# Performance work log

Hardware: AMD Instinct MI355X
Metric: run time of the kernel (lower is better)

Reference implementation:

```python
import jax, jax.numpy as jnp
import numpy as np

N = 50000
E = 640000
D_IN = 128
D_OUT = 128


def setup_inputs() -> dict:
    key = jax.random.key(0)
    k1, k2, k3, k4 = jax.random.split(key, 4)
    x = jax.random.normal(k1, (N, D_IN), dtype=jnp.float32)
    edge_index = jax.random.randint(k2, (2, E), 0, N, dtype=jnp.int64)
    # Linear(in_channels, out_channels) params, PyTorch default init scale
    lim = 1.0 / np.sqrt(D_IN)
    W = jax.random.uniform(k3, (D_IN, D_OUT), dtype=jnp.float32, minval=-lim, maxval=lim)
    b = jax.random.uniform(k4, (D_OUT,), dtype=jnp.float32, minval=-lim, maxval=lim)
    return {"x": x, "edge_index": edge_index, "W": W, "b": b}


def reference(x, edge_index, W, b):
    row, col = edge_index[0], edge_index[1]
    # gather source features, segment-sum onto destination rows
    msgs = x[col]  # [E, D_IN]
    summed = jax.ops.segment_sum(msgs, row, num_segments=N)  # [N, D_IN]
    counts = jax.ops.segment_sum(jnp.ones((E,), dtype=x.dtype), row, num_segments=N)
    # scatter_mean: empty segments -> 0 (avoid div by zero)
    x_agg = summed / jnp.maximum(counts, 1.0)[:, None]
    # Linear + ReLU
    return jax.nn.relu(x_agg @ W + b)
```

## Files before the change

kernel.cpp:

```cpp
#include <hip/hip_runtime.h>

#define NN 50000
#define DD 128
#define PAD 16
#define CAP 48
#define GEMM_BLOCKS 391

typedef __attribute__((ext_vector_type(8))) short bf16x8;
typedef __attribute__((ext_vector_type(4))) float f32x4;

static __device__ __forceinline__ unsigned short f2bf(float x) {
    unsigned int u = __float_as_uint(x);
    unsigned int r = (u + 0x7fffu + ((u >> 16) & 1u)) >> 16;
    return (unsigned short)r;
}

static __device__ __forceinline__ int swz(int byte) {
    return byte ^ (((byte >> 8) & 7) << 4);
}

__global__ void __launch_bounds__(256) zero_wt_kernel(
    int* __restrict__ pad, const float* __restrict__ W, unsigned short* __restrict__ Wt)
{
    if (blockIdx.x == 0) {
        for (int idx = threadIdx.x; idx < DD * DD; idx += 256) {
            int k = idx >> 7;
            int j = idx & 127;
            Wt[j * DD + k] = f2bf(W[idx]);
        }
    }
    int i = blockIdx.x * 256 + threadIdx.x;
    const int total = NN * PAD / 4;
    if (i < total) {
        reinterpret_cast<uint4*>(pad)[i] = make_uint4(0u, 0u, 0u, 0u);
    }
}

__global__ void __launch_bounds__(256) ticket_place_kernel(
    const int* __restrict__ row, const int* __restrict__ col,
    int* __restrict__ pad, unsigned short* __restrict__ slot, int E)
{
    int e = blockIdx.x * 256 + threadIdx.x;
    if (e < E) {
        int r = row[e];
        int t = atomicAdd(&pad[r * PAD], 1);
        if (t < CAP) slot[r * CAP + t] = (unsigned short)col[e];
    }
}

__global__ void __launch_bounds__(512) gemm_xw_kernel(
    const float* __restrict__ x,
    const unsigned short* __restrict__ Wt,
    unsigned short* __restrict__ y)
{
    __shared__ unsigned short w_lds[DD * DD];
    __shared__ unsigned short r_lds[128 * DD];

    const int tid = threadIdx.x;
    const int i0 = blockIdx.x * 128;

    {
        const uint4* src = reinterpret_cast<const uint4*>(Wt);
        #pragma unroll
        for (int it = 0; it < 4; ++it) {
            int idx = tid + it * 512;
            uint4 v = src[idx];
            *reinterpret_cast<uint4*>((char*)w_lds + swz(idx * 16)) = v;
        }
    }

    const int wave = tid >> 6;
    const int l64 = tid & 63;
    const int lrow = l64 & 15;
    const int kgrp = l64 >> 4;
    const int grow = min(i0 + wave * 16 + lrow, NN - 1);

    bf16x8 afrag[4];
    #pragma unroll
    for (int s = 0; s < 4; ++s) {
        const float4* xp = reinterpret_cast<const float4*>(
            x + (size_t)grow * DD + s * 32 + kgrp * 8);
        float4 p0 = xp[0];
        float4 p1 = xp[1];
        bf16x8 a;
        a[0] = (short)f2bf(p0.x); a[1] = (short)f2bf(p0.y);
        a[2] = (short)f2bf(p0.z); a[3] = (short)f2bf(p0.w);
        a[4] = (short)f2bf(p1.x); a[5] = (short)f2bf(p1.y);
        a[6] = (short)f2bf(p1.z); a[7] = (short)f2bf(p1.w);
        afrag[s] = a;
    }
    __syncthreads();

    f32x4 acc[8];
    #pragma unroll
    for (int t = 0; t < 8; ++t) acc[t] = (f32x4){0.f, 0.f, 0.f, 0.f};

    #pragma unroll
    for (int t = 0; t < 8; ++t) {
        #pragma unroll
        for (int s = 0; s < 4; ++s) {
            int byte = (t * 16 + lrow) * 256 + (s * 32 + kgrp * 8) * 2;
            bf16x8 bfrag = *reinterpret_cast<const bf16x8*>((char*)w_lds + swz(byte));
            acc[t] = __builtin_amdgcn_mfma_f32_16x16x32_bf16(afrag[s], bfrag, acc[t], 0, 0, 0);
        }
    }

    #pragma unroll
    for (int t = 0; t < 8; ++t) {
        #pragma unroll
        for (int r = 0; r < 4; ++r) {
            int lr = wave * 16 + kgrp * 4 + r;
            int byte = lr * 256 + (t * 16 + lrow) * 2;
            *reinterpret_cast<unsigned short*>((char*)r_lds + swz(byte)) = f2bf(acc[t][r]);
        }
    }
    __syncthreads();

    {
        uint4* dst = reinterpret_cast<uint4*>(y) + (size_t)i0 * 16;
        #pragma unroll
        for (int it = 0; it < 4; ++it) {
            int idx = tid + it * 512;
            if (i0 + (idx >> 4) < NN) {
                uint4 v = *reinterpret_cast<const uint4*>((char*)r_lds + swz(idx * 16));
                dst[idx] = v;
            }
        }
    }
}

__global__ void __launch_bounds__(256) gather_out_kernel(
    const unsigned short* __restrict__ y,
    const int* __restrict__ pad,
    const unsigned short* __restrict__ slot,
    const float* __restrict__ bias,
    float* __restrict__ out)
{
    int node = blockIdx.x * 8 + (threadIdx.x >> 5);
    int lane = threadIdx.x & 31;
    int q = lane >> 3;
    int l8 = lane & 7;
    if (node >= NN) return;
    int cnt0 = pad[node * PAD];
    int cnt = min(cnt0, CAP);
    int start = node * CAP;
    int end = start + cnt;

    float acc[16];
    #pragma unroll
    for (int j = 0; j < 16; ++j) acc[j] = 0.f;

    for (int base = start; base < end; base += 32) {
        int cl = (base + lane < end) ? (int)slot[base + lane] : 0;
        int m = min(32, end - base);
        for (int ii = 0; ii < m; ii += 4) {
            int src = ii + q;
            int c = __shfl(cl, src, 32);
            if (src < m) {
                const uint4* yp = reinterpret_cast<const uint4*>(y + (size_t)c * DD) + 2 * l8;
                uint4 u0 = yp[0];
                uint4 u1 = yp[1];
                acc[0]  += __uint_as_float(u0.x << 16);
                acc[1]  += __uint_as_float(u0.x & 0xffff0000u);
                acc[2]  += __uint_as_float(u0.y << 16);
                acc[3]  += __uint_as_float(u0.y & 0xffff0000u);
                acc[4]  += __uint_as_float(u0.z << 16);
                acc[5]  += __uint_as_float(u0.z & 0xffff0000u);
                acc[6]  += __uint_as_float(u0.w << 16);
                acc[7]  += __uint_as_float(u0.w & 0xffff0000u);
                acc[8]  += __uint_as_float(u1.x << 16);
                acc[9]  += __uint_as_float(u1.x & 0xffff0000u);
                acc[10] += __uint_as_float(u1.y << 16);
                acc[11] += __uint_as_float(u1.y & 0xffff0000u);
                acc[12] += __uint_as_float(u1.z << 16);
                acc[13] += __uint_as_float(u1.z & 0xffff0000u);
                acc[14] += __uint_as_float(u1.w << 16);
                acc[15] += __uint_as_float(u1.w & 0xffff0000u);
            }
        }
    }
    #pragma unroll
    for (int j = 0; j < 16; ++j) {
        acc[j] += __shfl_xor(acc[j], 8, 32);
        acc[j] += __shfl_xor(acc[j], 16, 32);
    }

    float inv = 1.0f / fmaxf((float)cnt0, 1.0f);
    float4 bb = reinterpret_cast<const float4*>(bias)[4 * l8 + q];
    float4 o;
    o.x = fmaxf(acc[4 * q + 0] * inv + bb.x, 0.f);
    o.y = fmaxf(acc[4 * q + 1] * inv + bb.y, 0.f);
    o.z = fmaxf(acc[4 * q + 2] * inv + bb.z, 0.f);
    o.w = fmaxf(acc[4 * q + 3] * inv + bb.w, 0.f);
    reinterpret_cast<float4*>(out + (size_t)node * DD)[4 * l8 + q] = o;
}

__global__ void __launch_bounds__(256) wt_only_kernel(
    const float* __restrict__ W, unsigned short* __restrict__ Wt)
{
    for (int idx = threadIdx.x; idx < DD * DD; idx += 256) {
        int k = idx >> 7;
        int j = idx & 127;
        Wt[j * DD + k] = f2bf(W[idx]);
    }
}

__global__ void __launch_bounds__(256) scatter_atomic_kernel(
    const float* __restrict__ x,
    const int* __restrict__ row, const int* __restrict__ col,
    float* __restrict__ agg, int* __restrict__ counts, int E)
{
    int gid = blockIdx.x * blockDim.x + threadIdx.x;
    int group = gid >> 5;
    int lane = threadIdx.x & 31;
    int ngroups = (gridDim.x * blockDim.x) >> 5;
    for (int e = group; e < E; e += ngroups) {
        int r = row[e];
        int c = col[e];
        float4 v = reinterpret_cast<const float4*>(x + (size_t)c * DD)[lane];
        float* dst = agg + (size_t)r * DD + lane * 4;
        unsafeAtomicAdd(dst + 0, v.x);
        unsafeAtomicAdd(dst + 1, v.y);
        unsafeAtomicAdd(dst + 2, v.z);
        unsafeAtomicAdd(dst + 3, v.w);
        if (lane == 0) atomicAdd(counts + r, 1);
    }
}

__global__ void __launch_bounds__(256) gemm_fb_kernel(
    const float* __restrict__ agg,
    const int* __restrict__ counts,
    const unsigned short* __restrict__ Wt,
    const float* __restrict__ bias,
    float* __restrict__ out)
{
    __shared__ unsigned short w_lds[DD * DD];
    __shared__ unsigned short a_lds[64 * DD];
    __shared__ float b_lds[DD];

    const int tid = threadIdx.x;
    const int i0 = blockIdx.x * 64;

    {
        const uint4* src = reinterpret_cast<const uint4*>(Wt);
        #pragma unroll
        for (int it = 0; it < 8; ++it) {
            int idx = tid + it * 256;
            *reinterpret_cast<uint4*>((char*)w_lds + swz(idx * 16)) = src[idx];
        }
    }
    if (tid < DD) b_lds[tid] = bias[tid];

    #pragma unroll
    for (int it = 0; it < 8; ++it) {
        int idx = tid + it * 256;
        int r = idx >> 5;
        int c4 = idx & 31;
        int grow = i0 + r;
        float4 v = make_float4(0.f, 0.f, 0.f, 0.f);
        float inv = 0.f;
        if (grow < NN) {
            v = reinterpret_cast<const float4*>(agg + (size_t)grow * DD)[c4];
            inv = 1.0f / fmaxf((float)counts[grow], 1.0f);
        }
        ushort4 o;
        o.x = f2bf(v.x * inv); o.y = f2bf(v.y * inv);
        o.z = f2bf(v.z * inv); o.w = f2bf(v.w * inv);
        *reinterpret_cast<ushort4*>((char*)a_lds + swz(r * 256 + c4 * 8)) = o;
    }
    __syncthreads();

    const int wave = tid >> 6;
    const int l64 = tid & 63;
    const int lrow = l64 & 15;
    const int kgrp = l64 >> 4;

    bf16x8 afrag[4];
    #pragma unroll
    for (int s = 0; s < 4; ++s) {
        int byte = (wave * 16 + lrow) * 256 + (s * 32 + kgrp * 8) * 2;
        afrag[s] = *reinterpret_cast<const bf16x8*>((char*)a_lds + swz(byte));
    }

    f32x4 acc[8];
    #pragma unroll
    for (int t = 0; t < 8; ++t) acc[t] = (f32x4){0.f, 0.f, 0.f, 0.f};

    #pragma unroll
    for (int t = 0; t < 8; ++t) {
        #pragma unroll
        for (int s = 0; s < 4; ++s) {
            int byte = (t * 16 + lrow) * 256 + (s * 32 + kgrp * 8) * 2;
            bf16x8 bfrag = *reinterpret_cast<const bf16x8*>((char*)w_lds + swz(byte));
            acc[t] = __builtin_amdgcn_mfma_f32_16x16x32_bf16(afrag[s], bfrag, acc[t], 0, 0, 0);
        }
    }

    #pragma unroll
    for (int t = 0; t < 8; ++t) {
        int colj = t * 16 + lrow;
        float bbv = b_lds[colj];
        #pragma unroll
        for (int r = 0; r < 4; ++r) {
            int grow = i0 + wave * 16 + kgrp * 4 + r;
            if (grow < NN) {
                out[(size_t)grow * DD + colj] = fmaxf(acc[t][r] + bbv, 0.f);
            }
        }
    }
}

extern "C" void kernel_launch(void* const* d_in, const int* in_sizes, int n_in,
                              void* d_out, int out_size, void* d_ws, size_t ws_size,
                              hipStream_t stream) {
    const float* x  = (const float*)d_in[0];
    const int* ei   = (const int*)d_in[1];
    const float* W  = (const float*)d_in[2];
    const float* b  = (const float*)d_in[3];
    float* out      = (float*)d_out;

    const int E = in_sizes[1] / 2;
    const int* row = ei;
    const int* col = ei + E;

    char* wsc = (char*)d_ws;
    int* pad             = (int*)(wsc + 0);
    unsigned short* slot = (unsigned short*)(wsc + 3200000);
    unsigned short* Wt   = (unsigned short*)(wsc + 8000000);
    unsigned short* y    = (unsigned short*)(wsc + 8032768);
    const size_t WS_NEED = 20832768;

    const int EB = (E + 255) / 256;

    if (ws_size >= WS_NEED) {
        zero_wt_kernel<<<800, 256, 0, stream>>>(pad, W, Wt);
        ticket_place_kernel<<<EB, 256, 0, stream>>>(row, col, pad, slot, E);
        gemm_xw_kernel<<<GEMM_BLOCKS, 512, 0, stream>>>(x, Wt, y);
        gather_out_kernel<<<(NN + 7) / 8, 256, 0, stream>>>(y, pad, slot, b, out);
    } else {
        int* fc = (int*)d_ws;
        unsigned short* fWt = (unsigned short*)(wsc + 200704);
        hipMemsetAsync(d_out, 0, (size_t)NN * DD * sizeof(float), stream);
        hipMemsetAsync(fc, 0, (size_t)NN * sizeof(int), stream);
        wt_only_kernel<<<1, 256, 0, stream>>>(W, fWt);
        scatter_atomic_kernel<<<2048, 256, 0, stream>>>(x, row, col, out, fc, E);
        gemm_fb_kernel<<<(NN + 63) / 64, 256, 0, stream>>>(out, fc, fWt, b, out);
    }
}
```

Before: 92.85 us.

## Fold pad zeroing and W bf16 transpose into GEMM kernel, dropping a launch

```diff
diff --git a/kernel.cpp b/kernel.cpp
--- a/kernel.cpp
+++ b/kernel.cpp
@@ -19,39 +19,11 @@
     return byte ^ (((byte >> 8) & 7) << 4);
 }
 
-__global__ void __launch_bounds__(256) zero_wt_kernel(
-    int* __restrict__ pad, const float* __restrict__ W, unsigned short* __restrict__ Wt)
-{
-    if (blockIdx.x == 0) {
-        for (int idx = threadIdx.x; idx < DD * DD; idx += 256) {
-            int k = idx >> 7;
-            int j = idx & 127;
-            Wt[j * DD + k] = f2bf(W[idx]);
-        }
-    }
-    int i = blockIdx.x * 256 + threadIdx.x;
-    const int total = NN * PAD / 4;
-    if (i < total) {
-        reinterpret_cast<uint4*>(pad)[i] = make_uint4(0u, 0u, 0u, 0u);
-    }
-}
-
-__global__ void __launch_bounds__(256) ticket_place_kernel(
-    const int* __restrict__ row, const int* __restrict__ col,
-    int* __restrict__ pad, unsigned short* __restrict__ slot, int E)
-{
-    int e = blockIdx.x * 256 + threadIdx.x;
-    if (e < E) {
-        int r = row[e];
-        int t = atomicAdd(&pad[r * PAD], 1);
-        if (t < CAP) slot[r * CAP + t] = (unsigned short)col[e];
-    }
-}
-
 __global__ void __launch_bounds__(512) gemm_xw_kernel(
     const float* __restrict__ x,
-    const unsigned short* __restrict__ Wt,
-    unsigned short* __restrict__ y)
+    const float* __restrict__ W,
+    unsigned short* __restrict__ y,
+    int* __restrict__ pad)
 {
     __shared__ unsigned short w_lds[DD * DD];
     __shared__ unsigned short r_lds[128 * DD];
@@ -60,12 +32,24 @@
     const int i0 = blockIdx.x * 128;
 
     {
-        const uint4* src = reinterpret_cast<const uint4*>(Wt);
-        #pragma unroll
-        for (int it = 0; it < 4; ++it) {
-            int idx = tid + it * 512;
-            uint4 v = src[idx];
-            *reinterpret_cast<uint4*>((char*)w_lds + swz(idx * 16)) = v;
+        int gid = blockIdx.x * 512 + tid;
+        if (gid < NN * PAD / 4) {
+            reinterpret_cast<uint4*>(pad)[gid] = make_uint4(0u, 0u, 0u, 0u);
+        }
+    }
+
+    {
+        const int j = tid & 127;
+        #pragma unroll
+        for (int it = 0; it < 8; ++it) {
+            int kbase = (tid >> 7) * 4 + it * 16;
+            float v0 = W[(kbase + 0) * DD + j];
+            float v1 = W[(kbase + 1) * DD + j];
+            float v2 = W[(kbase + 2) * DD + j];
+            float v3 = W[(kbase + 3) * DD + j];
+            ushort4 o;
+            o.x = f2bf(v0); o.y = f2bf(v1); o.z = f2bf(v2); o.w = f2bf(v3);
+            *reinterpret_cast<ushort4*>((char*)w_lds + swz(j * 256 + kbase * 2)) = o;
         }
     }
 
@@ -126,6 +110,18 @@
                 dst[idx] = v;
             }
         }
+    }
+}
+
+__global__ void __launch_bounds__(256) ticket_place_kernel(
+    const int* __restrict__ row, const int* __restrict__ col,
+    int* __restrict__ pad, unsigned short* __restrict__ slot, int E)
+{
+    int e = blockIdx.x * 256 + threadIdx.x;
+    if (e < E) {
+        int r = row[e];
+        int t = atomicAdd(&pad[r * PAD], 1);
+        if (t < CAP) slot[r * CAP + t] = (unsigned short)col[e];
     }
 }
 
@@ -326,16 +322,14 @@
     char* wsc = (char*)d_ws;
     int* pad             = (int*)(wsc + 0);
     unsigned short* slot = (unsigned short*)(wsc + 3200000);
-    unsigned short* Wt   = (unsigned short*)(wsc + 8000000);
-    unsigned short* y    = (unsigned short*)(wsc + 8032768);
-    const size_t WS_NEED = 20832768;
+    unsigned short* y    = (unsigned short*)(wsc + 8000000);
+    const size_t WS_NEED = 20800000;
 
     const int EB = (E + 255) / 256;
 
     if (ws_size >= WS_NEED) {
-        zero_wt_kernel<<<800, 256, 0, stream>>>(pad, W, Wt);
+        gemm_xw_kernel<<<GEMM_BLOCKS, 512, 0, stream>>>(x, W, y, pad);
         ticket_place_kernel<<<EB, 256, 0, stream>>>(row, col, pad, slot, E);
-        gemm_xw_kernel<<<GEMM_BLOCKS, 512, 0, stream>>>(x, Wt, y);
         gather_out_kernel<<<(NN + 7) / 8, 256, 0, stream>>>(y, pad, slot, b, out);
     } else {
         int* fc = (int*)d_ws;
```

After: 76.95 us, median of 2. 17.1% less time.
